# Kernel tuning notes

Measured on AMD Instinct MI355X. Metric: run time of the kernel, lower is better.

The kernel has to match this reference:

```python
import jax, jax.numpy as jnp
import numpy as np

S = 1024   # speakers_per_batch
U = 64     # utterances_per_speaker
E = 256    # model_embedding_size


def setup_inputs() -> dict:
    key = jax.random.key(0)
    k1, _ = jax.random.split(key)
    # embeds as produced by forward(): relu'd then L2-normalized rows
    raw = jax.nn.relu(jax.random.normal(k1, (S * U, E), dtype=jnp.float32))
    embeds = raw / (jnp.linalg.norm(raw, axis=1, keepdims=True) + 1e-12)
    return {
        "embeds": embeds,
        "similarity_weight": jnp.array([10.0], dtype=jnp.float32),
        "similarity_bias": jnp.array([-5.0], dtype=jnp.float32),
    }


def reference(embeds, similarity_weight, similarity_bias):
    e = embeds.reshape(S, U, E)                      # [S,U,E]
    # inclusive centroids (per speaker)
    c_incl = jnp.mean(e, axis=1)                     # [S,E]
    incl_norm = jnp.linalg.norm(c_incl, axis=1)      # [S]
    # exclusive centroids (leave-one-out per utterance)
    c_excl = (jnp.sum(e, axis=1, keepdims=True) - e) / (U - 1)  # [S,U,E]
    excl_norm = jnp.linalg.norm(c_excl, axis=2)      # [S,U]
    # off-diagonal (k != j): cosine vs inclusive centroid of speaker k
    sim = jnp.einsum('jue,ke->juk', e, c_incl) / incl_norm       # [S,U,S]
    # diagonal (k == j): cosine vs own exclusive centroid
    diag = jnp.einsum('jue,jue->ju', e, c_excl) / excl_norm      # [S,U]
    idx = jnp.arange(S)
    sim = sim.at[idx, :, idx].set(diag)
    sim = sim * similarity_weight[0] + similarity_bias[0]
    # cross-entropy against ground truth speaker ids
    logits = sim.reshape(S * U, S)                   # [SU,S]
    gt = jnp.repeat(jnp.arange(S), U)                # [SU]
    logp = jax.nn.log_softmax(logits, axis=-1)
    loss = -jnp.mean(jnp.take_along_axis(logp, gt[:, None], axis=1))
    preds = jnp.argmax(logits, axis=1)
    accuracy = jnp.mean((preds == gt).astype(jnp.float32))
    return loss, accuracy
```

## Files before the change

kernel.cpp:

```cpp
#include <hip/hip_runtime.h>
#include <math.h>

#define NS 1024
#define NU 64
#define NE 256

typedef __attribute__((ext_vector_type(4))) float f32x4;

__device__ static inline unsigned int pk4_fp8(float a, float b, float c,
                                              float d) {
  int r = 0;
  r = __builtin_amdgcn_cvt_pk_fp8_f32(a, b, r, false);
  r = __builtin_amdgcn_cvt_pk_fp8_f32(c, d, r, true);
  return (unsigned int)r;
}


__global__ __launch_bounds__(256) void centroid_kernel(
    const float* __restrict__ embeds, unsigned int* __restrict__ Cb,
    unsigned long long* __restrict__ Ab, float* __restrict__ normsum,
    float* __restrict__ ssumG, unsigned int* __restrict__ pmaxG,
    float* __restrict__ out) {
  int k = blockIdx.x;
  int t = threadIdx.x;
  if (t < 64) {
    ssumG[k * 64 + t] = 0.f;
    pmaxG[k * 64 + t] = 0u;
  }
  int wave = t >> 6, e4 = t & 63;

  const float4* base =
      (const float4*)(embeds + (size_t)k * NU * NE) + wave * 16 * 64 + e4;
  float4 s = {0.f, 0.f, 0.f, 0.f};
#pragma unroll
  for (int i = 0; i < 16; ++i) {
    float4 v = base[i * 64];
    s.x += v.x; s.y += v.y; s.z += v.z; s.w += v.w;
  }
  __shared__ float4 ps[4][64];
  ps[wave][e4] = s;
  __syncthreads();
  if (t < 64) {
    float4 a = ps[0][t], b = ps[1][t], c = ps[2][t], d = ps[3][t];
    float4 s4;
    s4.x = a.x + b.x + c.x + d.x;
    s4.y = a.y + b.y + c.y + d.y;
    s4.z = a.z + b.z + c.z + d.z;
    s4.w = a.w + b.w + c.w + d.w;
    float sq = s4.x * s4.x + s4.y * s4.y + s4.z * s4.z + s4.w * s4.w;
#pragma unroll
    for (int off = 32; off; off >>= 1) sq += __shfl_xor(sq, off, 64);
    float nrm = sqrtf(sq);
    float inv = 1.f / nrm;
    unsigned int v = pk4_fp8(s4.x * inv, s4.y * inv, s4.z * inv, s4.w * inv);
    int idx = (k >> 4) * 1024 + (t >> 3) * 128 +
              ((((t >> 1) & 3) * 16 + (k & 15)) << 1) + (t & 1);
    Cb[idx] = v;
    if (t == 0) {
      normsum[k] = nrm;
      if (k == 0) { out[0] = 0.f; out[1] = 0.f; }
    }
  }

  {
    int tile = t >> 6;
    int l = t & 63;
    int m = l & 15, qq = l >> 4;
    const float* rowp = embeds + (size_t)(k * 64 + tile * 16 + m) * NE;
    size_t basei = ((size_t)k * 4 + tile) * 512 + l;
#pragma unroll
    for (int sI = 0; sI < 8; ++sI) {
      int k0 = sI * 32 + qq * 8;
      float4 x = *(const float4*)(rowp + k0);
      float4 y = *(const float4*)(rowp + k0 + 4);
      unsigned int lo = pk4_fp8(x.x, x.y, x.z, x.w);
      unsigned int hi = pk4_fp8(y.x, y.y, y.z, y.w);
      Ab[basei + sI * 64] = ((unsigned long long)hi << 32) | lo;
    }
  }
}

__global__ __launch_bounds__(256, 2) void main_kernel(
    const long* __restrict__ Ab, const long* __restrict__ Cb,
    const float* __restrict__ normsum, const float* __restrict__ wp,
    const float* __restrict__ bp, float* __restrict__ ssumG,
    unsigned int* __restrict__ pmaxG, float* __restrict__ pdiagG) {
  int t = threadIdx.x;
  int wave = t >> 6, lane = t & 63;
  int c = lane & 15, q = lane >> 4;
  int b = blockIdx.x;
  int rg = b >> 1;
  int h = b & 1;
  int jspk = rg * 2 + (wave >> 1);
  int r0 = rg * 128 + wave * 32;

  float w = *wp, bia = *bp;
  const float L2E = 1.4426950408889634f;
  float M0 = fabsf(w) + bia;
  float wl = w * L2E;
  float cl = (bia - M0) * L2E;
  float ns = normsum[jspk];

  int fb = h * 32 * 512 + lane;

  long bfA[4], bfB[4];
#pragma unroll
  for (int s = 0; s < 4; ++s) bfA[s] = Cb[fb + s * 64];
#pragma unroll
  for (int s = 0; s < 4; ++s) bfB[s] = Cb[fb + (4 + s) * 64];

  long af[2][8];
#pragma unroll
  for (int mt = 0; mt < 2; ++mt) {
    int ab = ((r0 >> 4) + mt) * 512 + lane;
#pragma unroll
    for (int s = 0; s < 8; ++s) af[mt][s] = Ab[ab + s * 64];
  }

  float ssum[2][4];
  float pm[2][4];
#pragma unroll
  for (int mt = 0; mt < 2; ++mt)
#pragma unroll
    for (int r = 0; r < 4; ++r) {
      ssum[mt][r] = 0.f;
      pm[mt][r] = 0.f;
    }

#pragma unroll 1
  for (int T = 0; T < 32; ++T) {
    f32x4 acc[2];
    acc[0] = (f32x4){0.f, 0.f, 0.f, 0.f};
    acc[1] = (f32x4){0.f, 0.f, 0.f, 0.f};
    int nb = fb + (T + 1) * 512;
    bool more = (T + 1 < 32);
#pragma unroll
    for (int s = 0; s < 4; ++s) {
      acc[0] = __builtin_amdgcn_mfma_f32_16x16x32_fp8_fp8(af[0][s], bfA[s],
                                                          acc[0], 0, 0, 0);
      acc[1] = __builtin_amdgcn_mfma_f32_16x16x32_fp8_fp8(af[1][s], bfA[s],
                                                          acc[1], 0, 0, 0);
    }
    if (more) {
#pragma unroll
      for (int s = 0; s < 4; ++s) bfA[s] = Cb[nb + s * 64];
    }
#pragma unroll
    for (int s = 0; s < 4; ++s) {
      acc[0] = __builtin_amdgcn_mfma_f32_16x16x32_fp8_fp8(af[0][4 + s], bfB[s],
                                                          acc[0], 0, 0, 0);
      acc[1] = __builtin_amdgcn_mfma_f32_16x16x32_fp8_fp8(af[1][4 + s], bfB[s],
                                                          acc[1], 0, 0, 0);
    }
    if (more) {
#pragma unroll
      for (int s = 0; s < 4; ++s) bfB[s] = Cb[nb + (4 + s) * 64];
    }

    int gt = h * 32 + T;
    bool diagstep = ((jspk >> 4) == gt);
#pragma unroll
    for (int mt = 0; mt < 2; ++mt) {
      f32x4 a = acc[mt];
      if (diagstep && c == (jspk & 15)) {
#pragma unroll
        for (int r = 0; r < 4; ++r) {
          float Sv = a[r] * ns;
          float den = fmaxf(fmaf(ns, ns, 1.f) - 2.f * Sv, 1e-30f);
          float val = (Sv - 1.f) * __frsqrt_rn(den);
          float pd = exp2f(fmaf(val, wl, cl));
          pdiagG[r0 + mt * 16 + q * 4 + r] = pd;
          a[r] = val;
        }
      }
#pragma unroll
      for (int r = 0; r < 4; ++r) {
        float p = exp2f(fmaf(a[r], wl, cl));
        ssum[mt][r] += p;
        pm[mt][r] = fmaxf(pm[mt][r], p);
      }
    }
  }

#pragma unroll
  for (int mt = 0; mt < 2; ++mt)
#pragma unroll
    for (int r = 0; r < 4; ++r) {
      float s = ssum[mt][r];
      s += __shfl_xor(s, 1, 64);
      s += __shfl_xor(s, 2, 64);
      s += __shfl_xor(s, 4, 64);
      s += __shfl_xor(s, 8, 64);
      float m = pm[mt][r];
      m = fmaxf(m, __shfl_xor(m, 1, 64));
      m = fmaxf(m, __shfl_xor(m, 2, 64));
      m = fmaxf(m, __shfl_xor(m, 4, 64));
      m = fmaxf(m, __shfl_xor(m, 8, 64));
      if (c == 0) {
        int row = r0 + mt * 16 + q * 4 + r;
        atomicAdd(&ssumG[row], s);
        atomicMax(&pmaxG[row], __float_as_uint(m));
      }
    }
}

__global__ __launch_bounds__(256) void reduce_kernel(
    const float* __restrict__ ssumG, const unsigned int* __restrict__ pmaxG,
    const float* __restrict__ pdiagG, float* __restrict__ out) {
  int i = blockIdx.x * 256 + threadIdx.x;
  float pd = pdiagG[i];
  float lossr = __logf(ssumG[i] / pd);
  float corr = (pd >= __uint_as_float(pmaxG[i])) ? 1.f : 0.f;
#pragma unroll
  for (int off = 32; off; off >>= 1) {
    lossr += __shfl_xor(lossr, off, 64);
    corr += __shfl_xor(corr, off, 64);
  }
  __shared__ float pl[4], pc[4];
  int wave = threadIdx.x >> 6, lane = threadIdx.x & 63;
  if (lane == 0) { pl[wave] = lossr; pc[wave] = corr; }
  __syncthreads();
  if (threadIdx.x == 0) {
    const float inv = 1.f / (float)(NS * NU);
    atomicAdd(&out[0], (pl[0] + pl[1] + pl[2] + pl[3]) * inv);
    atomicAdd(&out[1], (pc[0] + pc[1] + pc[2] + pc[3]) * inv);
  }
}

extern "C" void kernel_launch(void* const* d_in, const int* in_sizes, int n_in,
                              void* d_out, int out_size, void* d_ws,
                              size_t ws_size, hipStream_t stream) {
  const float* embeds = (const float*)d_in[0];
  const float* w = (const float*)d_in[1];
  const float* b = (const float*)d_in[2];
  float* out = (float*)d_out;
  char* ws = (char*)d_ws;
  unsigned int* Cb = (unsigned int*)ws;
  unsigned int* pmaxG = (unsigned int*)(ws + (256 << 10));
  float* ssumG = (float*)(ws + (512 << 10));
  float* pdiagG = (float*)(ws + (768 << 10));
  float* normsum = (float*)(ws + (1024 << 10));
  unsigned long long* Ab =
      (unsigned long long*)(ws + (1056 << 10));

  centroid_kernel<<<NS, 256, 0, stream>>>(embeds, Cb, Ab, normsum, ssumG,
                                          pmaxG, out);
  main_kernel<<<1024, 256, 0, stream>>>((const long*)Ab, (const long*)Cb,
                                        normsum, w, b, ssumG, pmaxG, pdiagG);
  reduce_kernel<<<NS * NU / 256, 256, 0, stream>>>(ssumG, pmaxG, pdiagG, out);
}
```

Baseline: 149.8 us.

## Fuse final reduction into main kernel and double-buffer centroid tile loads

Removes the separate reduce kernel: each main-kernel block increments a per-row-group counter after its atomics, and the last of the two blocks for that row group computes the loss and accuracy contribution and adds it to the output. The inner loop is also restructured to process two column tiles per iteration with whole-tile prefetch into alternating register buffers (bfC/bfN), so each MFMA chain has its full B operand ready in advance. This saves a kernel launch and gives more room to overlap loads with compute, at the cost of more registers, an extra threadfence and counter atomics.

```diff
diff --git a/kernel.cpp b/kernel.cpp
--- a/kernel.cpp
+++ b/kernel.cpp
@@ -20,13 +20,14 @@
     const float* __restrict__ embeds, unsigned int* __restrict__ Cb,
     unsigned long long* __restrict__ Ab, float* __restrict__ normsum,
     float* __restrict__ ssumG, unsigned int* __restrict__ pmaxG,
-    float* __restrict__ out) {
+    unsigned int* __restrict__ cnt, float* __restrict__ out) {
   int k = blockIdx.x;
   int t = threadIdx.x;
   if (t < 64) {
     ssumG[k * 64 + t] = 0.f;
     pmaxG[k * 64 + t] = 0u;
   }
+  if (t == 0 && k < 512) cnt[k] = 0u;
   int wave = t >> 6, e4 = t & 63;
 
   const float4* base =
@@ -84,7 +85,8 @@
     const long* __restrict__ Ab, const long* __restrict__ Cb,
     const float* __restrict__ normsum, const float* __restrict__ wp,
     const float* __restrict__ bp, float* __restrict__ ssumG,
-    unsigned int* __restrict__ pmaxG, float* __restrict__ pdiagG) {
+    unsigned int* __restrict__ pmaxG, float* __restrict__ pdiagG,
+    unsigned int* __restrict__ cnt, float* __restrict__ out) {
   int t = threadIdx.x;
   int wave = t >> 6, lane = t & 63;
   int c = lane & 15, q = lane >> 4;
@@ -103,11 +105,9 @@
 
   int fb = h * 32 * 512 + lane;
 
-  long bfA[4], bfB[4];
-#pragma unroll
-  for (int s = 0; s < 4; ++s) bfA[s] = Cb[fb + s * 64];
-#pragma unroll
-  for (int s = 0; s < 4; ++s) bfB[s] = Cb[fb + (4 + s) * 64];
+  long bfC[8], bfN[8];
+#pragma unroll
+  for (int s = 0; s < 8; ++s) bfC[s] = Cb[fb + s * 64];
 
   long af[2][8];
 #pragma unroll
@@ -127,41 +127,13 @@
       pm[mt][r] = 0.f;
     }
 
-#pragma unroll 1
-  for (int T = 0; T < 32; ++T) {
-    f32x4 acc[2];
-    acc[0] = (f32x4){0.f, 0.f, 0.f, 0.f};
-    acc[1] = (f32x4){0.f, 0.f, 0.f, 0.f};
-    int nb = fb + (T + 1) * 512;
-    bool more = (T + 1 < 32);
-#pragma unroll
-    for (int s = 0; s < 4; ++s) {
-      acc[0] = __builtin_amdgcn_mfma_f32_16x16x32_fp8_fp8(af[0][s], bfA[s],
-                                                          acc[0], 0, 0, 0);
-      acc[1] = __builtin_amdgcn_mfma_f32_16x16x32_fp8_fp8(af[1][s], bfA[s],
-                                                          acc[1], 0, 0, 0);
-    }
-    if (more) {
-#pragma unroll
-      for (int s = 0; s < 4; ++s) bfA[s] = Cb[nb + s * 64];
-    }
-#pragma unroll
-    for (int s = 0; s < 4; ++s) {
-      acc[0] = __builtin_amdgcn_mfma_f32_16x16x32_fp8_fp8(af[0][4 + s], bfB[s],
-                                                          acc[0], 0, 0, 0);
-      acc[1] = __builtin_amdgcn_mfma_f32_16x16x32_fp8_fp8(af[1][4 + s], bfB[s],
-                                                          acc[1], 0, 0, 0);
-    }
-    if (more) {
-#pragma unroll
-      for (int s = 0; s < 4; ++s) bfB[s] = Cb[nb + (4 + s) * 64];
-    }
-
+  auto epilogue = [&](int T, f32x4 a0, f32x4 a1) {
     int gt = h * 32 + T;
     bool diagstep = ((jspk >> 4) == gt);
+    f32x4 av[2] = {a0, a1};
 #pragma unroll
     for (int mt = 0; mt < 2; ++mt) {
-      f32x4 a = acc[mt];
+      f32x4 a = av[mt];
       if (diagstep && c == (jspk & 15)) {
 #pragma unroll
         for (int r = 0; r < 4; ++r) {
@@ -180,6 +152,39 @@
         pm[mt][r] = fmaxf(pm[mt][r], p);
       }
     }
+  };
+
+#pragma unroll 1
+  for (int T = 0; T < 32; T += 2) {
+#pragma unroll
+    for (int s = 0; s < 8; ++s) bfN[s] = Cb[fb + (T + 1) * 512 + s * 64];
+
+    f32x4 acc0 = {0.f, 0.f, 0.f, 0.f};
+    f32x4 acc1 = {0.f, 0.f, 0.f, 0.f};
+#pragma unroll
+    for (int s = 0; s < 8; ++s) {
+      acc0 = __builtin_amdgcn_mfma_f32_16x16x32_fp8_fp8(af[0][s], bfC[s],
+                                                        acc0, 0, 0, 0);
+      acc1 = __builtin_amdgcn_mfma_f32_16x16x32_fp8_fp8(af[1][s], bfC[s],
+                                                        acc1, 0, 0, 0);
+    }
+    epilogue(T, acc0, acc1);
+
+    if (T + 2 < 32) {
+#pragma unroll
+      for (int s = 0; s < 8; ++s) bfC[s] = Cb[fb + (T + 2) * 512 + s * 64];
+    }
+
+    f32x4 acc2 = {0.f, 0.f, 0.f, 0.f};
+    f32x4 acc3 = {0.f, 0.f, 0.f, 0.f};
+#pragma unroll
+    for (int s = 0; s < 8; ++s) {
+      acc2 = __builtin_amdgcn_mfma_f32_16x16x32_fp8_fp8(af[0][s], bfN[s],
+                                                        acc2, 0, 0, 0);
+      acc3 = __builtin_amdgcn_mfma_f32_16x16x32_fp8_fp8(af[1][s], bfN[s],
+                                                        acc3, 0, 0, 0);
+    }
+    epilogue(T + 1, acc2, acc3);
   }
 
 #pragma unroll
@@ -202,28 +207,32 @@
         atomicMax(&pmaxG[row], __float_as_uint(m));
       }
     }
-}
-
-__global__ __launch_bounds__(256) void reduce_kernel(
-    const float* __restrict__ ssumG, const unsigned int* __restrict__ pmaxG,
-    const float* __restrict__ pdiagG, float* __restrict__ out) {
-  int i = blockIdx.x * 256 + threadIdx.x;
-  float pd = pdiagG[i];
-  float lossr = __logf(ssumG[i] / pd);
-  float corr = (pd >= __uint_as_float(pmaxG[i])) ? 1.f : 0.f;
-#pragma unroll
-  for (int off = 32; off; off >>= 1) {
-    lossr += __shfl_xor(lossr, off, 64);
-    corr += __shfl_xor(corr, off, 64);
-  }
-  __shared__ float pl[4], pc[4];
-  int wave = threadIdx.x >> 6, lane = threadIdx.x & 63;
-  if (lane == 0) { pl[wave] = lossr; pc[wave] = corr; }
+
+  __threadfence();
+  __shared__ unsigned int lastflag;
+  __shared__ float pl[2], pc[2];
+  if (t == 0) lastflag = atomicAdd(&cnt[rg], 1u);
   __syncthreads();
-  if (threadIdx.x == 0) {
-    const float inv = 1.f / (float)(NS * NU);
-    atomicAdd(&out[0], (pl[0] + pl[1] + pl[2] + pl[3]) * inv);
-    atomicAdd(&out[1], (pc[0] + pc[1] + pc[2] + pc[3]) * inv);
+  if (lastflag == 1u) {
+    __threadfence();
+    if (t < 128) {
+      int i = rg * 128 + t;
+      float pd = pdiagG[i];
+      float lossr = __logf(ssumG[i] / pd);
+      float corr = (pd >= __uint_as_float(pmaxG[i])) ? 1.f : 0.f;
+#pragma unroll
+      for (int off = 32; off; off >>= 1) {
+        lossr += __shfl_xor(lossr, off, 64);
+        corr += __shfl_xor(corr, off, 64);
+      }
+      if (lane == 0) { pl[wave] = lossr; pc[wave] = corr; }
+    }
+    __syncthreads();
+    if (t == 0) {
+      const float inv = 1.f / (float)(NS * NU);
+      atomicAdd(&out[0], (pl[0] + pl[1]) * inv);
+      atomicAdd(&out[1], (pc[0] + pc[1]) * inv);
+    }
   }
 }
 
@@ -240,12 +249,13 @@
   float* ssumG = (float*)(ws + (512 << 10));
   float* pdiagG = (float*)(ws + (768 << 10));
   float* normsum = (float*)(ws + (1024 << 10));
+  unsigned int* cnt = (unsigned int*)(ws + (1028 << 10));
   unsigned long long* Ab =
       (unsigned long long*)(ws + (1056 << 10));
 
   centroid_kernel<<<NS, 256, 0, stream>>>(embeds, Cb, Ab, normsum, ssumG,
-                                          pmaxG, out);
+                                          pmaxG, cnt, out);
   main_kernel<<<1024, 256, 0, stream>>>((const long*)Ab, (const long*)Cb,
-                                        normsum, w, b, ssumG, pmaxG, pdiagG);
-  reduce_kernel<<<NS * NU / 256, 256, 0, stream>>>(ssumG, pmaxG, pdiagG, out);
-}
+                                        normsum, w, b, ssumG, pmaxG, pdiagG,
+                                        cnt, out);
+}
```

Measured after the change: 241.6 us. 1.61x slower.
